# Kernel tuning notes

Measured on AMD Instinct MI355X. Metric: run time of the kernel, lower is better.

Reference implementation:

```python
import jax, jax.numpy as jnp
import numpy as np

N, E, F, H, L, G, C = 50000, 800000, 64, 128, 4, 64, 10
GAMMA = 10.0  # Gaussian RBF width for centers in (0,1)
CENTERS = jnp.linspace(0.0, 1.0, H)


def _ssp(v):
    # shifted softplus, SchNet's nonlinearity
    return jax.nn.softplus(v) - 0.6931472


def setup_inputs() -> dict:
    key = jax.random.key(0)
    ks = jax.random.split(key, 20)

    def w(k, shape, fan_in):
        return (jax.random.normal(k, shape, dtype=jnp.float32) / np.sqrt(fan_in)).astype(jnp.float32)

    x = jax.random.normal(ks[0], (N, F), dtype=jnp.float32)
    edge_dist = jax.random.uniform(ks[1], (E,), dtype=jnp.float32)
    edge_src = jax.random.randint(ks[2], (E,), 0, N, dtype=jnp.int32)
    edge_dst = jax.random.randint(ks[3], (E,), 0, N, dtype=jnp.int32)
    graph_ids = jnp.sort(jax.random.randint(ks[4], (N,), 0, G, dtype=jnp.int32))

    return {
        "x": x, "edge_dist": edge_dist,
        "edge_src": edge_src, "edge_dst": edge_dst, "graph_ids": graph_ids,
        # first-layer node projection F->H, remaining layers H->H (stacked)
        "W1_0": w(ks[5], (F, H), F), "b1_0": jnp.zeros((H,), jnp.float32),
        "W1_rest": w(ks[6], (L - 1, H, H), H), "b1_rest": jnp.zeros((L - 1, H), jnp.float32),
        # filter-generating MLP on RBF features, per layer
        "Wf1": w(ks[7], (L, H, H), H), "bf1": jnp.zeros((L, H), jnp.float32),
        "Wf2": w(ks[8], (L, H, H), H), "bf2": jnp.zeros((L, H), jnp.float32),
        # output projection per layer
        "W2": w(ks[9], (L, H, H), H), "b2": jnp.zeros((L, H), jnp.float32),
        # readout FC
        "fc_w": w(ks[10], (H, C), H), "fc_b": jnp.zeros((C,), jnp.float32),
    }


def _schnet_conv(x, rbf, src, dst, W1, b1, Wf1, bf1, Wf2, bf2, W2, b2):
    # CFConv: project nodes, gate gathered source features with a distance
    # filter, scatter-sum to destinations, project out.
    filt = _ssp(rbf @ Wf1 + bf1) @ Wf2 + bf2          # [E, H]
    h = x @ W1 + b1                                    # [N, H]
    msg = h[src] * filt                                # [E, H] gather + gate
    agg = jax.ops.segment_sum(msg, dst, num_segments=N)  # [N, H] scatter-sum
    return agg @ W2 + b2


def reference(x, edge_dist, edge_src, edge_dst, graph_ids,
              W1_0, b1_0, W1_rest, b1_rest, Wf1, bf1, Wf2, bf2, W2, b2,
              fc_w, fc_b):
    # Gaussian radial basis expansion of edge distances, shared across layers
    rbf = jnp.exp(-GAMMA * (edge_dist[:, None] - CENTERS) ** 2)  # [E, H]

    h = jax.nn.relu(_schnet_conv(x, rbf, edge_src, edge_dst,
                                 W1_0, b1_0, Wf1[0], bf1[0], Wf2[0], bf2[0],
                                 W2[0], b2[0]))
    for i in range(L - 1):
        h = jax.nn.relu(_schnet_conv(h, rbf, edge_src, edge_dst,
                                     W1_rest[i], b1_rest[i],
                                     Wf1[i + 1], bf1[i + 1],
                                     Wf2[i + 1], bf2[i + 1],
                                     W2[i + 1], b2[i + 1]))

    # dgl.mean_nodes: per-graph mean over nodes
    sums = jax.ops.segment_sum(h, graph_ids, num_segments=G)           # [G, H]
    cnts = jax.ops.segment_sum(jnp.ones((N,), h.dtype), graph_ids, num_segments=G)
    pooled = sums / jnp.maximum(cnts, 1.0)[:, None]

    logits = pooled @ fc_w + fc_b                                       # [G, C]
    return jax.nn.log_softmax(logits, axis=1)
```

## Files before the change

### kernel.cpp

```cpp
#include <hip/hip_runtime.h>
#include <math.h>

#define NN 50000
#define EE 800000
#define FF 64
#define HH 128
#define LL 4
#define GG 64
#define CC 10
#define TT 512
#define BD 64
#define ABLK 1024
#define EPB 782
#define SEGC 192
#define SUBB 96
#define SRW 6250

#define PB_CVTW 8
#define PB_TAB ((TT / 16) * LL)
#define PB_CVTX (NN * FF / 4 / 256)
#define PB_PART ABLK

typedef unsigned short ushort_t;
typedef unsigned int uint_t;

typedef short s8v __attribute__((ext_vector_type(8)));
typedef float f32x4 __attribute__((ext_vector_type(4)));

__device__ inline ushort_t f2bf(float f) {
  uint_t u = __float_as_uint(f);
  uint_t r = (u + 0x7FFFu + ((u >> 16) & 1u)) >> 16;
  return (ushort_t)r;
}
__device__ inline float bf_lo(uint_t pair) { return __uint_as_float(pair << 16); }
__device__ inline float bf_hi(uint_t pair) { return __uint_as_float(pair & 0xFFFF0000u); }
__device__ inline float bf1f(ushort_t v) { return __uint_as_float(((uint_t)v) << 16); }

__global__ __launch_bounds__(256) void prep(
    const float* __restrict__ x, ushort_t* __restrict__ xb,
    const float* __restrict__ W1_0, const float* __restrict__ W1_rest,
    const float* __restrict__ W2, ushort_t* __restrict__ wt,
    const float* __restrict__ Wf1, const float* __restrict__ bf1,
    const float* __restrict__ Wf2, const float* __restrict__ bf2,
    ushort_t* __restrict__ tables,
    const int* __restrict__ dst, const int* __restrict__ src,
    const float* __restrict__ dist,
    uint2* __restrict__ seg, int* __restrict__ segcnt, int* __restrict__ bcnt,
    const int* __restrict__ gid, int* __restrict__ gcnt, float* __restrict__ gsum) {
  __shared__ float rbf[16][HH];
  __shared__ float hid[16][HH];
  __shared__ int lcnt[8];
  int tid = threadIdx.x;
  int b = blockIdx.x;

  if (b < PB_CVTW) {
    int mid = b;
    const float* srcm; int K;
    if (mid == 0) { srcm = W1_0; K = FF; }
    else if (mid < 4) { srcm = W1_rest + (size_t)(mid - 1) * HH * HH; K = HH; }
    else { srcm = W2 + (size_t)(mid - 4) * HH * HH; K = HH; }
    ushort_t* dstm = wt + (size_t)mid * HH * HH;
    for (int idx = tid; idx < K * HH; idx += 256) {
      int k = idx >> 7, n = idx & 127;
      dstm[n * K + k] = f2bf(srcm[idx]);
    }
  } else if (b < PB_CVTW + PB_TAB) {
    int bb = b - PB_CVTW;
    int l = bb & 3;
    int tb = (bb >> 2) * 16;
    int j = tid & 127;
    float c = j * (1.0f / (HH - 1));
#pragma unroll
    for (int tt2 = 0; tt2 < 16; ++tt2) {
      float d = (tb + tt2) * (1.0f / (TT - 1));
      float dd = d - c;
      rbf[tt2][j] = expf(-10.0f * dd * dd);
    }
    __syncthreads();
    const float* W1f = Wf1 + (size_t)l * HH * HH;
    float s[16];
    float bb1 = bf1[l * HH + j];
#pragma unroll
    for (int tt2 = 0; tt2 < 16; ++tt2) s[tt2] = bb1;
    for (int k = 0; k < HH; ++k) {
      float wk = W1f[(size_t)k * HH + j];
#pragma unroll
      for (int tt2 = 0; tt2 < 16; ++tt2) s[tt2] += rbf[tt2][k] * wk;
    }
#pragma unroll
    for (int tt2 = 0; tt2 < 16; ++tt2)
      hid[tt2][j] = fmaxf(s[tt2], 0.f) + log1pf(expf(-fabsf(s[tt2]))) - 0.6931472f;
    __syncthreads();
    const float* W2f = Wf2 + (size_t)l * HH * HH;
    float bb2 = bf2[l * HH + j];
#pragma unroll
    for (int tt2 = 0; tt2 < 16; ++tt2) s[tt2] = bb2;
    for (int k = 0; k < HH; ++k) {
      float wk = W2f[(size_t)k * HH + j];
#pragma unroll
      for (int tt2 = 0; tt2 < 16; ++tt2) s[tt2] += hid[tt2][k] * wk;
    }
    if (tid < 128) {
#pragma unroll
      for (int tt2 = 0; tt2 < 16; ++tt2)
        tables[((size_t)l * TT + tb + tt2) * HH + j] = f2bf(s[tt2]);
    }
  } else if (b < PB_CVTW + PB_TAB + PB_CVTX) {
    int i = (b - PB_CVTW - PB_TAB) * 256 + tid;
    const float4* x4 = (const float4*)x;
    float4 v = x4[i];
    union { ushort_t us[4]; uint2 u; } pk;
    pk.us[0] = f2bf(v.x); pk.us[1] = f2bf(v.y); pk.us[2] = f2bf(v.z); pk.us[3] = f2bf(v.w);
    *(uint2*)&xb[i * 4] = pk.u;
  } else if (b < PB_CVTW + PB_TAB + PB_CVTX + PB_PART) {
    int pb = b - PB_CVTW - PB_TAB - PB_CVTX;
    if (tid < 8) lcnt[tid] = 0;
    int z = pb * 49 + tid;
    if (tid < 49 && z < NN) bcnt[z] = 0;
    __syncthreads();
    int e0 = pb * EPB;
    int e1 = min(e0 + EPB, EE);
    for (int e = e0 + tid; e < e1; e += 256) {
      int d = __builtin_nontemporal_load(dst + e);
      int s = __builtin_nontemporal_load(src + e);
      float di = __builtin_nontemporal_load(dist + e);
      float u = di * (float)(TT - 1);
      int t0 = (int)(fminf(fmaxf(u, 0.f), (float)(TT - 1)) + 0.5f);
      if (t0 > TT - 1) t0 = TT - 1;
      int r = d / SRW;
      int pos = atomicAdd(&lcnt[r], 1);
      if (pos < SEGC)
        seg[((size_t)(r << 10) + pb) * SEGC + pos] =
            make_uint2((uint_t)d, ((uint_t)s << 9) | (uint_t)t0);
    }
    __syncthreads();
    if (tid < 8) segcnt[(tid << 10) + pb] = min(lcnt[tid], SEGC);
  } else {
    for (int i = tid; i < GG * HH; i += 256) gsum[i] = 0.f;
    if (tid < GG) {
      int g = tid;
      int lo = 0, hi = NN;
      while (lo < hi) { int m = (lo + hi) >> 1; if (gid[m] < g) lo = m + 1; else hi = m; }
      int b0 = lo;
      lo = 0; hi = NN;
      int g1 = g + 1;
      while (lo < hi) { int m = (lo + hi) >> 1; if (gid[m] < g1) lo = m + 1; else hi = m; }
      gcnt[g] = lo - b0;
    }
  }
}

__global__ __launch_bounds__(256) void scatter_edges(
    const uint2* __restrict__ seg, const int* __restrict__ segcnt,
    int* __restrict__ bcnt, uint_t* __restrict__ epad) {
  int r = blockIdx.x & 7;
  int sub = blockIdx.x >> 3;
  int tid = threadIdx.x;
  for (int b = sub; b < ABLK; b += SUBB) {
    int cnt = segcnt[(r << 10) + b];
    const uint_t* sp = (const uint_t*)(seg + ((size_t)(r << 10) + b) * SEGC);
    for (int i = tid; i < cnt; i += 256) {
      uint_t ex = __builtin_nontemporal_load(sp + i * 2);
      uint_t ey = __builtin_nontemporal_load(sp + i * 2 + 1);
      int slot = atomicAdd(&bcnt[ex], 1);
      if (slot < BD) epad[(size_t)ex * BD + slot] = ey;
    }
  }
}

__global__ __launch_bounds__(256) void gemm_mfma(
    const ushort_t* __restrict__ A, const ushort_t* __restrict__ WT,
    const float* __restrict__ bias, ushort_t* __restrict__ OUT,
    int K, int act) {
  int lane = threadIdx.x & 63;
  int wave = threadIdx.x >> 6;
  int m = lane & 15;
  int quad = lane >> 4;
  int rowbase = blockIdx.x * 16;
  int colbase = wave * 32;
  const ushort_t* arow = A + (size_t)(rowbase + m) * K;
  const ushort_t* brow0 = WT + (size_t)(colbase + m) * K;
  const ushort_t* brow1 = WT + (size_t)(colbase + 16 + m) * K;
  f32x4 acc0 = {0.f, 0.f, 0.f, 0.f};
  f32x4 acc1 = {0.f, 0.f, 0.f, 0.f};
  for (int kc = 0; kc < K; kc += 32) {
    int k = kc + quad * 8;
    union { uint4 u; s8v v; } a, b0, b1;
    a.u  = *(const uint4*)(arow + k);
    b0.u = *(const uint4*)(brow0 + k);
    b1.u = *(const uint4*)(brow1 + k);
    acc0 = __builtin_amdgcn_mfma_f32_16x16x32_bf16(a.v, b0.v, acc0, 0, 0, 0);
    acc1 = __builtin_amdgcn_mfma_f32_16x16x32_bf16(a.v, b1.v, acc1, 0, 0, 0);
  }
  float bb0 = bias[colbase + m];
  float bb1 = bias[colbase + 16 + m];
#pragma unroll
  for (int reg = 0; reg < 4; ++reg) {
    int row = rowbase + quad * 4 + reg;
    float v0 = acc0[reg] + bb0;
    float v1 = acc1[reg] + bb1;
    if (act) { v0 = fmaxf(v0, 0.f); v1 = fmaxf(v1, 0.f); }
    OUT[(size_t)row * HH + colbase + m] = f2bf(v0);
    OUT[(size_t)row * HH + colbase + 16 + m] = f2bf(v1);
  }
}

__global__ __launch_bounds__(256) void gemm2_mfma(
    const ushort_t* __restrict__ AGG,
    const ushort_t* __restrict__ WT2, const float* __restrict__ b2l,
    const ushort_t* __restrict__ WT1, const float* __restrict__ b1l,
    ushort_t* __restrict__ OUT) {
  __shared__ ushort_t T[16 * 128];
  int lane = threadIdx.x & 63;
  int wave = threadIdx.x >> 6;
  int m = lane & 15;
  int quad = lane >> 4;
  int rowbase = blockIdx.x * 16;
  int colbase = wave * 32;
  {
    const ushort_t* arow = AGG + (size_t)(rowbase + m) * HH;
    const ushort_t* brow0 = WT2 + (size_t)(colbase + m) * HH;
    const ushort_t* brow1 = WT2 + (size_t)(colbase + 16 + m) * HH;
    f32x4 acc0 = {0.f, 0.f, 0.f, 0.f};
    f32x4 acc1 = {0.f, 0.f, 0.f, 0.f};
    for (int kc = 0; kc < HH; kc += 32) {
      int k = kc + quad * 8;
      union { uint4 u; s8v v; } a, b0, b1;
      a.u  = *(const uint4*)(arow + k);
      b0.u = *(const uint4*)(brow0 + k);
      b1.u = *(const uint4*)(brow1 + k);
      acc0 = __builtin_amdgcn_mfma_f32_16x16x32_bf16(a.v, b0.v, acc0, 0, 0, 0);
      acc1 = __builtin_amdgcn_mfma_f32_16x16x32_bf16(a.v, b1.v, acc1, 0, 0, 0);
    }
    float bb0 = b2l[colbase + m];
    float bb1 = b2l[colbase + 16 + m];
#pragma unroll
    for (int reg = 0; reg < 4; ++reg) {
      int r = quad * 4 + reg;
      float v0 = fmaxf(acc0[reg] + bb0, 0.f);
      float v1 = fmaxf(acc1[reg] + bb1, 0.f);
      int c0 = colbase + m, c1 = colbase + 16 + m;
      T[r * 128 + (((c0 >> 3) ^ r) << 3) + (c0 & 7)] = f2bf(v0);
      T[r * 128 + (((c1 >> 3) ^ r) << 3) + (c1 & 7)] = f2bf(v1);
    }
  }
  __syncthreads();
  {
    const ushort_t* brow0 = WT1 + (size_t)(colbase + m) * HH;
    const ushort_t* brow1 = WT1 + (size_t)(colbase + 16 + m) * HH;
    f32x4 acc0 = {0.f, 0.f, 0.f, 0.f};
    f32x4 acc1 = {0.f, 0.f, 0.f, 0.f};
    for (int kc = 0; kc < HH; kc += 32) {
      int k0 = kc + quad * 8;
      int g = k0 >> 3;
      union { uint4 u; s8v v; } a, b0, b1;
      a.u = *(const uint4*)&T[m * 128 + ((g ^ m) << 3)];
      b0.u = *(const uint4*)(brow0 + k0);
      b1.u = *(const uint4*)(brow1 + k0);
      acc0 = __builtin_amdgcn_mfma_f32_16x16x32_bf16(a.v, b0.v, acc0, 0, 0, 0);
      acc1 = __builtin_amdgcn_mfma_f32_16x16x32_bf16(a.v, b1.v, acc1, 0, 0, 0);
    }
    float bb0 = b1l[colbase + m];
    float bb1 = b1l[colbase + 16 + m];
#pragma unroll
    for (int reg = 0; reg < 4; ++reg) {
      int row = rowbase + quad * 4 + reg;
      OUT[(size_t)row * HH + colbase + m] = f2bf(acc0[reg] + bb0);
      OUT[(size_t)row * HH + colbase + 16 + m] = f2bf(acc1[reg] + bb1);
    }
  }
}

__global__ __launch_bounds__(256) void edge_agg(
    const ushort_t* __restrict__ p, const ushort_t* __restrict__ table,
    const uint_t* __restrict__ epad, const int* __restrict__ bcnt,
    ushort_t* __restrict__ agg) {
  int v = (blockIdx.x << 2) + (threadIdx.x >> 6);
  int lane = threadIdx.x & 63;
  if (v >= NN) return;
  int n = min(bcnt[v], BD);
  uint_t ed = (lane < n) ? epad[(size_t)v * BD + lane] : 0u;
  float ax = 0.f, ay = 0.f;
  int i = 0;
  int n4 = n & ~3;
  for (; i < n4; i += 4) {
    uint_t e0 = __shfl(ed, i + 0), e1 = __shfl(ed, i + 1);
    uint_t e2 = __shfl(ed, i + 2), e3 = __shfl(ed, i + 3);
    const uint_t* P0 = (const uint_t*)(p + (size_t)(e0 >> 9) * HH);
    const uint_t* P1 = (const uint_t*)(p + (size_t)(e1 >> 9) * HH);
    const uint_t* P2 = (const uint_t*)(p + (size_t)(e2 >> 9) * HH);
    const uint_t* P3 = (const uint_t*)(p + (size_t)(e3 >> 9) * HH);
    const uint_t* T0 = (const uint_t*)(table + (size_t)(e0 & 511u) * HH);
    const uint_t* T1 = (const uint_t*)(table + (size_t)(e1 & 511u) * HH);
    const uint_t* T2 = (const uint_t*)(table + (size_t)(e2 & 511u) * HH);
    const uint_t* T3 = (const uint_t*)(table + (size_t)(e3 & 511u) * HH);
    uint_t pv0 = P0[lane], pv1 = P1[lane], pv2 = P2[lane], pv3 = P3[lane];
    uint_t f0 = T0[lane], f1 = T1[lane], f2 = T2[lane], f3 = T3[lane];
    ax += bf_lo(pv0) * bf_lo(f0); ay += bf_hi(pv0) * bf_hi(f0);
    ax += bf_lo(pv1) * bf_lo(f1); ay += bf_hi(pv1) * bf_hi(f1);
    ax += bf_lo(pv2) * bf_lo(f2); ay += bf_hi(pv2) * bf_hi(f2);
    ax += bf_lo(pv3) * bf_lo(f3); ay += bf_hi(pv3) * bf_hi(f3);
  }
  for (; i < n; ++i) {
    uint_t e = __shfl(ed, i);
    uint_t pv = ((const uint_t*)(p + (size_t)(e >> 9) * HH))[lane];
    uint_t f = ((const uint_t*)(table + (size_t)(e & 511u) * HH))[lane];
    ax += bf_lo(pv) * bf_lo(f);
    ay += bf_hi(pv) * bf_hi(f);
  }
  uint_t packed = (uint_t)f2bf(ax) | ((uint_t)f2bf(ay) << 16);
  ((uint_t*)agg)[(size_t)v * 64 + lane] = packed;
}

__global__ __launch_bounds__(128) void pool_kernel(const ushort_t* __restrict__ h, const int* __restrict__ gid,
                                                   float* __restrict__ gsum) {
  int j = threadIdx.x;
  int i0 = blockIdx.x * 128;
  int i1 = min(i0 + 128, NN);
  if (i0 >= NN) return;
  float acc = 0.f;
  int gcur = gid[i0];
  for (int i = i0; i < i1; ++i) {
    int g = gid[i];
    if (g != gcur) {
      atomicAdd(&gsum[gcur * HH + j], acc);
      acc = 0.f;
      gcur = g;
    }
    acc += bf1f(h[(size_t)i * HH + j]);
  }
  atomicAdd(&gsum[gcur * HH + j], acc);
}

__global__ __launch_bounds__(128) void final_kernel(const float* __restrict__ gsum, const int* __restrict__ gcnt,
                                                    const float* __restrict__ fc_w, const float* __restrict__ fc_b,
                                                    float* __restrict__ out) {
  int g = blockIdx.x, j = threadIdx.x;
  __shared__ float pooled[HH];
  __shared__ float logits[CC];
  __shared__ float lse;
  float cnt = fmaxf((float)gcnt[g], 1.0f);
  pooled[j] = gsum[g * HH + j] / cnt;
  __syncthreads();
  if (j < CC) {
    float s = fc_b[j];
    for (int k = 0; k < HH; ++k) s += pooled[k] * fc_w[k * CC + j];
    logits[j] = s;
  }
  __syncthreads();
  if (j == 0) {
    float m = -1e30f;
    for (int c = 0; c < CC; ++c) m = fmaxf(m, logits[c]);
    float s = 0.f;
    for (int c = 0; c < CC; ++c) s += expf(logits[c] - m);
    lse = m + logf(s);
  }
  __syncthreads();
  if (j < CC) out[g * CC + j] = logits[j] - lse;
}

extern "C" void kernel_launch(void* const* d_in, const int* in_sizes, int n_in,
                              void* d_out, int out_size, void* d_ws, size_t ws_size,
                              hipStream_t stream) {
  const float* x       = (const float*)d_in[0];
  const float* edist   = (const float*)d_in[1];
  const int*   esrc    = (const int*)d_in[2];
  const int*   edst    = (const int*)d_in[3];
  const int*   gid     = (const int*)d_in[4];
  const float* W1_0    = (const float*)d_in[5];
  const float* b1_0    = (const float*)d_in[6];
  const float* W1_rest = (const float*)d_in[7];
  const float* b1_rest = (const float*)d_in[8];
  const float* Wf1     = (const float*)d_in[9];
  const float* bf1     = (const float*)d_in[10];
  const float* Wf2     = (const float*)d_in[11];
  const float* bf2     = (const float*)d_in[12];
  const float* W2      = (const float*)d_in[13];
  const float* b2      = (const float*)d_in[14];
  const float* fc_w    = (const float*)d_in[15];
  const float* fc_b    = (const float*)d_in[16];
  float* out = (float*)d_out;

  char* ws = (char*)d_ws;
  size_t o = 0;
  auto alloc = [&](size_t bytes) {
    void* p = ws + o;
    o += (bytes + 255) & ~(size_t)255;
    return p;
  };
  ushort_t* tables = (ushort_t*)alloc(sizeof(ushort_t) * (size_t)LL * TT * HH);
  ushort_t* xb     = (ushort_t*)alloc(sizeof(ushort_t) * (size_t)NN * FF);
  ushort_t* wt     = (ushort_t*)alloc(sizeof(ushort_t) * 8 * HH * HH);
  ushort_t* pbuf   = (ushort_t*)alloc(sizeof(ushort_t) * (size_t)NN * HH);
  ushort_t* hbuf   = (ushort_t*)alloc(sizeof(ushort_t) * (size_t)NN * HH);
  ushort_t* aggbuf = (ushort_t*)alloc(sizeof(ushort_t) * (size_t)NN * HH);
  int*      bcnt   = (int*)alloc(sizeof(int) * NN);
  uint_t*   epad   = (uint_t*)alloc(sizeof(uint_t) * (size_t)NN * BD);
  uint2*    seg    = (uint2*)alloc(sizeof(uint2) * (size_t)8 * ABLK * SEGC);
  int*      segcnt = (int*)alloc(sizeof(int) * 8 * ABLK);
  float*    gsum   = (float*)alloc(sizeof(float) * GG * HH);
  int*      gcnt   = (int*)alloc(sizeof(int) * GG);

  const int prepBlocks = PB_CVTW + PB_TAB + PB_CVTX + PB_PART + 1;
  prep<<<prepBlocks, 256, 0, stream>>>(x, xb, W1_0, W1_rest, W2, wt,
                                       Wf1, bf1, Wf2, bf2, tables,
                                       edst, esrc, edist, seg, segcnt, bcnt,
                                       gid, gcnt, gsum);
  scatter_edges<<<8 * SUBB, 256, 0, stream>>>(seg, segcnt, bcnt, epad);

  const int gemmBlocks = NN / 16;
  gemm_mfma<<<gemmBlocks, 256, 0, stream>>>(xb, wt, b1_0, pbuf, FF, 0);
  for (int l = 0; l < LL; ++l) {
    edge_agg<<<(NN + 3) / 4, 256, 0, stream>>>(pbuf, tables + (size_t)l * TT * HH,
                                               epad, bcnt, aggbuf);
    if (l < LL - 1) {
      gemm2_mfma<<<gemmBlocks, 256, 0, stream>>>(aggbuf,
                                                 wt + (size_t)(4 + l) * HH * HH, b2 + (size_t)l * HH,
                                                 wt + (size_t)(1 + l) * HH * HH, b1_rest + (size_t)l * HH,
                                                 pbuf);
    } else {
      gemm_mfma<<<gemmBlocks, 256, 0, stream>>>(aggbuf, wt + (size_t)(4 + l) * HH * HH,
                                                b2 + (size_t)l * HH, hbuf, HH, 1);
    }
  }

  pool_kernel<<<(NN + 127) / 128, 128, 0, stream>>>(hbuf, gid, gsum);
  final_kernel<<<GG, 128, 0, stream>>>(gsum, gcnt, fc_w, fc_b, out);
}
```

Baseline: 463.3 us.

## Fuse all stages into one persistent cooperative kernel with grid-wide syncs

Result: slower. 1.453 ms (+213.6%).

```diff
diff --git a/kernel.cpp b/kernel.cpp
--- a/kernel.cpp
+++ b/kernel.cpp
@@ -1,5 +1,8 @@
 #include <hip/hip_runtime.h>
+#include <hip/hip_cooperative_groups.h>
 #include <math.h>
+
+namespace cg = cooperative_groups;
 
 #define NN 50000
 #define EE 800000
@@ -20,6 +23,7 @@
 #define PB_TAB ((TT / 16) * LL)
 #define PB_CVTX (NN * FF / 4 / 256)
 #define PB_PART ABLK
+#define PB_TOTAL (PB_CVTW + PB_TAB + PB_CVTX + PB_PART + 1)
 
 typedef unsigned short ushort_t;
 typedef unsigned int uint_t;
@@ -36,23 +40,20 @@
 __device__ inline float bf_hi(uint_t pair) { return __uint_as_float(pair & 0xFFFF0000u); }
 __device__ inline float bf1f(ushort_t v) { return __uint_as_float(((uint_t)v) << 16); }
 
-__global__ __launch_bounds__(256) void prep(
+
+__device__ inline void prep_block(
+    int b, int tid,
     const float* __restrict__ x, ushort_t* __restrict__ xb,
     const float* __restrict__ W1_0, const float* __restrict__ W1_rest,
     const float* __restrict__ W2, ushort_t* __restrict__ wt,
     const float* __restrict__ Wf1, const float* __restrict__ bf1,
     const float* __restrict__ Wf2, const float* __restrict__ bf2,
     ushort_t* __restrict__ tables,
-    const int* __restrict__ dst, const int* __restrict__ src,
-    const float* __restrict__ dist,
+    const int* __restrict__ edst, const int* __restrict__ esrc,
+    const float* __restrict__ edist,
     uint2* __restrict__ seg, int* __restrict__ segcnt, int* __restrict__ bcnt,
-    const int* __restrict__ gid, int* __restrict__ gcnt, float* __restrict__ gsum) {
-  __shared__ float rbf[16][HH];
-  __shared__ float hid[16][HH];
-  __shared__ int lcnt[8];
-  int tid = threadIdx.x;
-  int b = blockIdx.x;
-
+    const int* __restrict__ gid, int* __restrict__ gcnt, float* __restrict__ gsum,
+    float (*rbf)[HH], float (*hid)[HH], int* lcnt) {
   if (b < PB_CVTW) {
     int mid = b;
     const float* srcm; int K;
@@ -71,39 +72,39 @@
     int j = tid & 127;
     float c = j * (1.0f / (HH - 1));
 #pragma unroll
-    for (int tt2 = 0; tt2 < 16; ++tt2) {
-      float d = (tb + tt2) * (1.0f / (TT - 1));
+    for (int t2 = 0; t2 < 16; ++t2) {
+      float d = (tb + t2) * (1.0f / (TT - 1));
       float dd = d - c;
-      rbf[tt2][j] = expf(-10.0f * dd * dd);
+      rbf[t2][j] = expf(-10.0f * dd * dd);
     }
     __syncthreads();
     const float* W1f = Wf1 + (size_t)l * HH * HH;
     float s[16];
     float bb1 = bf1[l * HH + j];
 #pragma unroll
-    for (int tt2 = 0; tt2 < 16; ++tt2) s[tt2] = bb1;
+    for (int t2 = 0; t2 < 16; ++t2) s[t2] = bb1;
     for (int k = 0; k < HH; ++k) {
       float wk = W1f[(size_t)k * HH + j];
 #pragma unroll
-      for (int tt2 = 0; tt2 < 16; ++tt2) s[tt2] += rbf[tt2][k] * wk;
-    }
-#pragma unroll
-    for (int tt2 = 0; tt2 < 16; ++tt2)
-      hid[tt2][j] = fmaxf(s[tt2], 0.f) + log1pf(expf(-fabsf(s[tt2]))) - 0.6931472f;
+      for (int t2 = 0; t2 < 16; ++t2) s[t2] += rbf[t2][k] * wk;
+    }
+#pragma unroll
+    for (int t2 = 0; t2 < 16; ++t2)
+      hid[t2][j] = fmaxf(s[t2], 0.f) + log1pf(expf(-fabsf(s[t2]))) - 0.6931472f;
     __syncthreads();
     const float* W2f = Wf2 + (size_t)l * HH * HH;
     float bb2 = bf2[l * HH + j];
 #pragma unroll
-    for (int tt2 = 0; tt2 < 16; ++tt2) s[tt2] = bb2;
+    for (int t2 = 0; t2 < 16; ++t2) s[t2] = bb2;
     for (int k = 0; k < HH; ++k) {
       float wk = W2f[(size_t)k * HH + j];
 #pragma unroll
-      for (int tt2 = 0; tt2 < 16; ++tt2) s[tt2] += hid[tt2][k] * wk;
+      for (int t2 = 0; t2 < 16; ++t2) s[t2] += hid[t2][k] * wk;
     }
     if (tid < 128) {
 #pragma unroll
-      for (int tt2 = 0; tt2 < 16; ++tt2)
-        tables[((size_t)l * TT + tb + tt2) * HH + j] = f2bf(s[tt2]);
+      for (int t2 = 0; t2 < 16; ++t2)
+        tables[((size_t)l * TT + tb + t2) * HH + j] = f2bf(s[t2]);
     }
   } else if (b < PB_CVTW + PB_TAB + PB_CVTX) {
     int i = (b - PB_CVTW - PB_TAB) * 256 + tid;
@@ -121,9 +122,9 @@
     int e0 = pb * EPB;
     int e1 = min(e0 + EPB, EE);
     for (int e = e0 + tid; e < e1; e += 256) {
-      int d = __builtin_nontemporal_load(dst + e);
-      int s = __builtin_nontemporal_load(src + e);
-      float di = __builtin_nontemporal_load(dist + e);
+      int d = __builtin_nontemporal_load(edst + e);
+      int s = __builtin_nontemporal_load(esrc + e);
+      float di = __builtin_nontemporal_load(edist + e);
       float u = di * (float)(TT - 1);
       int t0 = (int)(fminf(fmaxf(u, 0.f), (float)(TT - 1)) + 0.5f);
       if (t0 > TT - 1) t0 = TT - 1;
@@ -150,34 +151,27 @@
   }
 }
 
-__global__ __launch_bounds__(256) void scatter_edges(
-    const uint2* __restrict__ seg, const int* __restrict__ segcnt,
+__device__ inline void scatter_vb(
+    int vb, int tid, const uint2* __restrict__ seg, const int* __restrict__ segcnt,
     int* __restrict__ bcnt, uint_t* __restrict__ epad) {
-  int r = blockIdx.x & 7;
-  int sub = blockIdx.x >> 3;
-  int tid = threadIdx.x;
-  for (int b = sub; b < ABLK; b += SUBB) {
-    int cnt = segcnt[(r << 10) + b];
-    const uint_t* sp = (const uint_t*)(seg + ((size_t)(r << 10) + b) * SEGC);
+  int r = vb & 7, sub = vb >> 3;
+  for (int bb = sub; bb < ABLK; bb += SUBB) {
+    int cnt = segcnt[(r << 10) + bb];
+    const uint_t* sp = (const uint_t*)(seg + ((size_t)(r << 10) + bb) * SEGC);
     for (int i = tid; i < cnt; i += 256) {
-      uint_t ex = __builtin_nontemporal_load(sp + i * 2);
-      uint_t ey = __builtin_nontemporal_load(sp + i * 2 + 1);
+      uint_t ex = sp[i * 2];
+      uint_t ey = sp[i * 2 + 1];
       int slot = atomicAdd(&bcnt[ex], 1);
       if (slot < BD) epad[(size_t)ex * BD + slot] = ey;
     }
   }
 }
 
-__global__ __launch_bounds__(256) void gemm_mfma(
-    const ushort_t* __restrict__ A, const ushort_t* __restrict__ WT,
-    const float* __restrict__ bias, ushort_t* __restrict__ OUT,
-    int K, int act) {
-  int lane = threadIdx.x & 63;
-  int wave = threadIdx.x >> 6;
-  int m = lane & 15;
-  int quad = lane >> 4;
-  int rowbase = blockIdx.x * 16;
-  int colbase = wave * 32;
+__device__ inline void gemm_tile(const ushort_t* __restrict__ A, const ushort_t* __restrict__ WT,
+                                 const float* __restrict__ bias, ushort_t* __restrict__ OUT,
+                                 int K, int act, int tile, int tid) {
+  int lane = tid & 63, wave = tid >> 6, m = lane & 15, quad = lane >> 4;
+  int rowbase = tile * 16, colbase = wave * 32;
   const ushort_t* arow = A + (size_t)(rowbase + m) * K;
   const ushort_t* brow0 = WT + (size_t)(colbase + m) * K;
   const ushort_t* brow1 = WT + (size_t)(colbase + 16 + m) * K;
@@ -205,18 +199,12 @@
   }
 }
 
-__global__ __launch_bounds__(256) void gemm2_mfma(
-    const ushort_t* __restrict__ AGG,
-    const ushort_t* __restrict__ WT2, const float* __restrict__ b2l,
-    const ushort_t* __restrict__ WT1, const float* __restrict__ b1l,
-    ushort_t* __restrict__ OUT) {
-  __shared__ ushort_t T[16 * 128];
-  int lane = threadIdx.x & 63;
-  int wave = threadIdx.x >> 6;
-  int m = lane & 15;
-  int quad = lane >> 4;
-  int rowbase = blockIdx.x * 16;
-  int colbase = wave * 32;
+__device__ inline void gemm2_tile(const ushort_t* __restrict__ AGG,
+                                  const ushort_t* __restrict__ WT2, const float* __restrict__ b2l,
+                                  const ushort_t* __restrict__ WT1, const float* __restrict__ b1l,
+                                  ushort_t* __restrict__ OUT, int tile, int tid, ushort_t* T) {
+  int lane = tid & 63, wave = tid >> 6, m = lane & 15, quad = lane >> 4;
+  int rowbase = tile * 16, colbase = wave * 32;
   {
     const ushort_t* arow = AGG + (size_t)(rowbase + m) * HH;
     const ushort_t* brow0 = WT2 + (size_t)(colbase + m) * HH;
@@ -269,14 +257,15 @@
       OUT[(size_t)row * HH + colbase + 16 + m] = f2bf(acc1[reg] + bb1);
     }
   }
-}
-
-__global__ __launch_bounds__(256) void edge_agg(
-    const ushort_t* __restrict__ p, const ushort_t* __restrict__ table,
+  __syncthreads();
+}
+
+__device__ inline void edge_group(
+    int vg, int tid, const ushort_t* __restrict__ p, const ushort_t* __restrict__ tab,
     const uint_t* __restrict__ epad, const int* __restrict__ bcnt,
     ushort_t* __restrict__ agg) {
-  int v = (blockIdx.x << 2) + (threadIdx.x >> 6);
-  int lane = threadIdx.x & 63;
+  int v = (vg << 2) + (tid >> 6);
+  int lane = tid & 63;
   if (v >= NN) return;
   int n = min(bcnt[v], BD);
   uint_t ed = (lane < n) ? epad[(size_t)v * BD + lane] : 0u;
@@ -290,10 +279,10 @@
     const uint_t* P1 = (const uint_t*)(p + (size_t)(e1 >> 9) * HH);
     const uint_t* P2 = (const uint_t*)(p + (size_t)(e2 >> 9) * HH);
     const uint_t* P3 = (const uint_t*)(p + (size_t)(e3 >> 9) * HH);
-    const uint_t* T0 = (const uint_t*)(table + (size_t)(e0 & 511u) * HH);
-    const uint_t* T1 = (const uint_t*)(table + (size_t)(e1 & 511u) * HH);
-    const uint_t* T2 = (const uint_t*)(table + (size_t)(e2 & 511u) * HH);
-    const uint_t* T3 = (const uint_t*)(table + (size_t)(e3 & 511u) * HH);
+    const uint_t* T0 = (const uint_t*)(tab + (size_t)(e0 & 511u) * HH);
+    const uint_t* T1 = (const uint_t*)(tab + (size_t)(e1 & 511u) * HH);
+    const uint_t* T2 = (const uint_t*)(tab + (size_t)(e2 & 511u) * HH);
+    const uint_t* T3 = (const uint_t*)(tab + (size_t)(e3 & 511u) * HH);
     uint_t pv0 = P0[lane], pv1 = P1[lane], pv2 = P2[lane], pv3 = P3[lane];
     uint_t f0 = T0[lane], f1 = T1[lane], f2 = T2[lane], f3 = T3[lane];
     ax += bf_lo(pv0) * bf_lo(f0); ay += bf_hi(pv0) * bf_hi(f0);
@@ -304,7 +293,7 @@
   for (; i < n; ++i) {
     uint_t e = __shfl(ed, i);
     uint_t pv = ((const uint_t*)(p + (size_t)(e >> 9) * HH))[lane];
-    uint_t f = ((const uint_t*)(table + (size_t)(e & 511u) * HH))[lane];
+    uint_t f = ((const uint_t*)(tab + (size_t)(e & 511u) * HH))[lane];
     ax += bf_lo(pv) * bf_lo(f);
     ay += bf_hi(pv) * bf_hi(f);
   }
@@ -312,12 +301,13 @@
   ((uint_t*)agg)[(size_t)v * 64 + lane] = packed;
 }
 
-__global__ __launch_bounds__(128) void pool_kernel(const ushort_t* __restrict__ h, const int* __restrict__ gid,
-                                                   float* __restrict__ gsum) {
-  int j = threadIdx.x;
-  int i0 = blockIdx.x * 128;
+__device__ inline void pool_vb(int vb, int tid, const ushort_t* __restrict__ h,
+                               const int* __restrict__ gid, float* __restrict__ gsum) {
+  int strip = vb * 2 + (tid >> 7);
+  int j = tid & 127;
+  int i0 = strip * 128;
+  if (i0 >= NN) return;
   int i1 = min(i0 + 128, NN);
-  if (i0 >= NN) return;
   float acc = 0.f;
   int gcur = gid[i0];
   for (int i = i0; i < i1; ++i) {
@@ -332,31 +322,148 @@
   atomicAdd(&gsum[gcur * HH + j], acc);
 }
 
-__global__ __launch_bounds__(128) void final_kernel(const float* __restrict__ gsum, const int* __restrict__ gcnt,
-                                                    const float* __restrict__ fc_w, const float* __restrict__ fc_b,
-                                                    float* __restrict__ out) {
-  int g = blockIdx.x, j = threadIdx.x;
+__device__ inline void final_graph(int g, int tid, const float* __restrict__ gsum,
+                                   const int* __restrict__ gcnt,
+                                   const float* __restrict__ fc_w, const float* __restrict__ fc_b,
+                                   float* __restrict__ out,
+                                   float* pooled, float* logits, float* lse) {
+  if (tid < HH) pooled[tid] = gsum[g * HH + tid] / fmaxf((float)gcnt[g], 1.0f);
+  __syncthreads();
+  if (tid < CC) {
+    float s = fc_b[tid];
+    for (int k = 0; k < HH; ++k) s += pooled[k] * fc_w[k * CC + tid];
+    logits[tid] = s;
+  }
+  __syncthreads();
+  if (tid == 0) {
+    float mx = -1e30f;
+    for (int c2 = 0; c2 < CC; ++c2) mx = fmaxf(mx, logits[c2]);
+    float s = 0.f;
+    for (int c2 = 0; c2 < CC; ++c2) s += expf(logits[c2] - mx);
+    *lse = mx + logf(s);
+  }
+  __syncthreads();
+  if (tid < CC) out[g * CC + tid] = logits[tid] - *lse;
+  __syncthreads();
+}
+
+__global__ __launch_bounds__(256, 4) void mega(
+    const float* __restrict__ x, ushort_t* __restrict__ xb,
+    const float* __restrict__ W1_0, const float* __restrict__ W1_rest,
+    const float* __restrict__ W2, ushort_t* __restrict__ wt,
+    const float* __restrict__ Wf1, const float* __restrict__ bf1,
+    const float* __restrict__ Wf2, const float* __restrict__ bf2,
+    ushort_t* __restrict__ tables,
+    const int* __restrict__ edst, const int* __restrict__ esrc,
+    const float* __restrict__ edist,
+    uint2* __restrict__ seg, int* __restrict__ segcnt, int* __restrict__ bcnt,
+    uint_t* __restrict__ epad,
+    const int* __restrict__ gid, int* __restrict__ gcnt, float* __restrict__ gsum,
+    ushort_t* __restrict__ pbuf, ushort_t* __restrict__ hbuf, ushort_t* __restrict__ aggbuf,
+    const float* __restrict__ b1_0, const float* __restrict__ b1_rest,
+    const float* __restrict__ b2,
+    const float* __restrict__ fc_w, const float* __restrict__ fc_b,
+    float* __restrict__ out) {
+  cg::grid_group grid = cg::this_grid();
+  const int tid = threadIdx.x;
+  const int nb = gridDim.x;
+
+  __shared__ union {
+    struct { float rbf[16][HH]; float hid[16][HH]; int lcnt[8]; } prep;
+    ushort_t T[16 * 128];
+    struct { float pooled[HH]; float logits[CC]; float lse; } fin;
+  } sh;
+
+  for (int b = blockIdx.x; b < PB_TOTAL; b += nb) {
+    prep_block(b, tid, x, xb, W1_0, W1_rest, W2, wt, Wf1, bf1, Wf2, bf2, tables,
+               edst, esrc, edist, seg, segcnt, bcnt, gid, gcnt, gsum,
+               sh.prep.rbf, sh.prep.hid, sh.prep.lcnt);
+    __syncthreads();
+  }
+  grid.sync();
+
+  for (int vb = blockIdx.x; vb < 8 * SUBB; vb += nb)
+    scatter_vb(vb, tid, seg, segcnt, bcnt, epad);
+  grid.sync();
+
+  for (int t = blockIdx.x; t < NN / 16; t += nb)
+    gemm_tile(xb, wt, b1_0, pbuf, FF, 0, t, tid);
+
+  for (int l = 0; l < LL; ++l) {
+    grid.sync();
+    const ushort_t* tab = tables + (size_t)l * TT * HH;
+    for (int vg = blockIdx.x; vg < (NN + 3) / 4; vg += nb)
+      edge_group(vg, tid, pbuf, tab, epad, bcnt, aggbuf);
+    grid.sync();
+    if (l < LL - 1) {
+      for (int t = blockIdx.x; t < NN / 16; t += nb)
+        gemm2_tile(aggbuf, wt + (size_t)(4 + l) * HH * HH, b2 + (size_t)l * HH,
+                   wt + (size_t)(1 + l) * HH * HH, b1_rest + (size_t)l * HH,
+                   pbuf, t, tid, sh.T);
+    } else {
+      for (int t = blockIdx.x; t < NN / 16; t += nb)
+        gemm_tile(aggbuf, wt + (size_t)(4 + l) * HH * HH, b2 + (size_t)l * HH,
+                  hbuf, HH, 1, t, tid);
+    }
+  }
+  grid.sync();
+
+  for (int vb = blockIdx.x; vb < 196; vb += nb)
+    pool_vb(vb, tid, hbuf, gid, gsum);
+  grid.sync();
+
+  for (int g = blockIdx.x; g < GG; g += nb)
+    final_graph(g, tid, gsum, gcnt, fc_w, fc_b, out,
+                sh.fin.pooled, sh.fin.logits, &sh.fin.lse);
+}
+
+__global__ __launch_bounds__(256) void k_prep(
+    const float* x, ushort_t* xb, const float* W1_0, const float* W1_rest,
+    const float* W2, ushort_t* wt, const float* Wf1, const float* bf1,
+    const float* Wf2, const float* bf2, ushort_t* tables,
+    const int* edst, const int* esrc, const float* edist,
+    uint2* seg, int* segcnt, int* bcnt,
+    const int* gid, int* gcnt, float* gsum) {
+  __shared__ float rbf[16][HH];
+  __shared__ float hid[16][HH];
+  __shared__ int lcnt[8];
+  prep_block(blockIdx.x, threadIdx.x, x, xb, W1_0, W1_rest, W2, wt, Wf1, bf1, Wf2, bf2,
+             tables, edst, esrc, edist, seg, segcnt, bcnt, gid, gcnt, gsum, rbf, hid, lcnt);
+}
+
+__global__ __launch_bounds__(256) void k_scatter(const uint2* seg, const int* segcnt,
+                                                 int* bcnt, uint_t* epad) {
+  scatter_vb(blockIdx.x, threadIdx.x, seg, segcnt, bcnt, epad);
+}
+
+__global__ __launch_bounds__(256) void k_gemm(const ushort_t* A, const ushort_t* WT,
+                                              const float* bias, ushort_t* OUT, int K, int act) {
+  gemm_tile(A, WT, bias, OUT, K, act, blockIdx.x, threadIdx.x);
+}
+
+__global__ __launch_bounds__(256) void k_gemm2(const ushort_t* AGG, const ushort_t* WT2,
+                                               const float* b2l, const ushort_t* WT1,
+                                               const float* b1l, ushort_t* OUT) {
+  __shared__ ushort_t T[16 * 128];
+  gemm2_tile(AGG, WT2, b2l, WT1, b1l, OUT, blockIdx.x, threadIdx.x, T);
+}
+
+__global__ __launch_bounds__(256) void k_edge(const ushort_t* p, const ushort_t* tab,
+                                              const uint_t* epad, const int* bcnt,
+                                              ushort_t* agg) {
+  edge_group(blockIdx.x, threadIdx.x, p, tab, epad, bcnt, agg);
+}
+
+__global__ __launch_bounds__(256) void k_pool(const ushort_t* h, const int* gid, float* gsum) {
+  pool_vb(blockIdx.x, threadIdx.x, h, gid, gsum);
+}
+
+__global__ __launch_bounds__(256) void k_final(const float* gsum, const int* gcnt,
+                                               const float* fc_w, const float* fc_b, float* out) {
   __shared__ float pooled[HH];
   __shared__ float logits[CC];
   __shared__ float lse;
-  float cnt = fmaxf((float)gcnt[g], 1.0f);
-  pooled[j] = gsum[g * HH + j] / cnt;
-  __syncthreads();
-  if (j < CC) {
-    float s = fc_b[j];
-    for (int k = 0; k < HH; ++k) s += pooled[k] * fc_w[k * CC + j];
-    logits[j] = s;
-  }
-  __syncthreads();
-  if (j == 0) {
-    float m = -1e30f;
-    for (int c = 0; c < CC; ++c) m = fmaxf(m, logits[c]);
-    float s = 0.f;
-    for (int c = 0; c < CC; ++c) s += expf(logits[c] - m);
-    lse = m + logf(s);
-  }
-  __syncthreads();
-  if (j < CC) out[g * CC + j] = logits[j] - lse;
+  final_graph(blockIdx.x, threadIdx.x, gsum, gcnt, fc_w, fc_b, out, pooled, logits, &lse);
 }
 
 extern "C" void kernel_launch(void* const* d_in, const int* in_sizes, int n_in,
@@ -401,29 +508,50 @@
   float*    gsum   = (float*)alloc(sizeof(float) * GG * HH);
   int*      gcnt   = (int*)alloc(sizeof(int) * GG);
 
-  const int prepBlocks = PB_CVTW + PB_TAB + PB_CVTX + PB_PART + 1;
-  prep<<<prepBlocks, 256, 0, stream>>>(x, xb, W1_0, W1_rest, W2, wt,
-                                       Wf1, bf1, Wf2, bf2, tables,
-                                       edst, esrc, edist, seg, segcnt, bcnt,
-                                       gid, gcnt, gsum);
-  scatter_edges<<<8 * SUBB, 256, 0, stream>>>(seg, segcnt, bcnt, epad);
-
-  const int gemmBlocks = NN / 16;
-  gemm_mfma<<<gemmBlocks, 256, 0, stream>>>(xb, wt, b1_0, pbuf, FF, 0);
-  for (int l = 0; l < LL; ++l) {
-    edge_agg<<<(NN + 3) / 4, 256, 0, stream>>>(pbuf, tables + (size_t)l * TT * HH,
+  int dev = 0;
+  (void)hipGetDevice(&dev);
+  int coopAttr = 0;
+  (void)hipDeviceGetAttribute(&coopAttr, hipDeviceAttributeCooperativeLaunch, dev);
+  int nCU = 0;
+  (void)hipDeviceGetAttribute(&nCU, hipDeviceAttributeMultiprocessorCount, dev);
+  int occ = 0;
+  (void)hipOccupancyMaxActiveBlocksPerMultiprocessor(&occ, mega, 256, 0);
+
+  if (coopAttr && occ >= 1 && nCU > 0) {
+    int gridN = occ * nCU;
+    if (gridN > 1024) gridN = 1024;
+    void* args[] = {
+      (void*)&x, (void*)&xb, (void*)&W1_0, (void*)&W1_rest, (void*)&W2, (void*)&wt,
+      (void*)&Wf1, (void*)&bf1, (void*)&Wf2, (void*)&bf2, (void*)&tables,
+      (void*)&edst, (void*)&esrc, (void*)&edist,
+      (void*)&seg, (void*)&segcnt, (void*)&bcnt, (void*)&epad,
+      (void*)&gid, (void*)&gcnt, (void*)&gsum,
+      (void*)&pbuf, (void*)&hbuf, (void*)&aggbuf,
+      (void*)&b1_0, (void*)&b1_rest, (void*)&b2,
+      (void*)&fc_w, (void*)&fc_b, (void*)&out
+    };
+    (void)hipLaunchCooperativeKernel(mega, dim3(gridN), dim3(256), (void**)args, 0, stream);
+  } else {
+    k_prep<<<PB_TOTAL, 256, 0, stream>>>(x, xb, W1_0, W1_rest, W2, wt, Wf1, bf1, Wf2, bf2,
+                                         tables, edst, esrc, edist, seg, segcnt, bcnt,
+                                         gid, gcnt, gsum);
+    k_scatter<<<8 * SUBB, 256, 0, stream>>>(seg, segcnt, bcnt, epad);
+    const int gemmBlocks = NN / 16;
+    k_gemm<<<gemmBlocks, 256, 0, stream>>>(xb, wt, b1_0, pbuf, FF, 0);
+    for (int l = 0; l < LL; ++l) {
+      k_edge<<<(NN + 3) / 4, 256, 0, stream>>>(pbuf, tables + (size_t)l * TT * HH,
                                                epad, bcnt, aggbuf);
-    if (l < LL - 1) {
-      gemm2_mfma<<<gemmBlocks, 256, 0, stream>>>(aggbuf,
-                                                 wt + (size_t)(4 + l) * HH * HH, b2 + (size_t)l * HH,
-                                                 wt + (size_t)(1 + l) * HH * HH, b1_rest + (size_t)l * HH,
-                                                 pbuf);
-    } else {
-      gemm_mfma<<<gemmBlocks, 256, 0, stream>>>(aggbuf, wt + (size_t)(4 + l) * HH * HH,
-                                                b2 + (size_t)l * HH, hbuf, HH, 1);
-    }
-  }
-
-  pool_kernel<<<(NN + 127) / 128, 128, 0, stream>>>(hbuf, gid, gsum);
-  final_kernel<<<GG, 128, 0, stream>>>(gsum, gcnt, fc_w, fc_b, out);
-}
+      if (l < LL - 1) {
+        k_gemm2<<<gemmBlocks, 256, 0, stream>>>(aggbuf,
+                                                wt + (size_t)(4 + l) * HH * HH, b2 + (size_t)l * HH,
+                                                wt + (size_t)(1 + l) * HH * HH, b1_rest + (size_t)l * HH,
+                                                pbuf);
+      } else {
+        k_gemm<<<gemmBlocks, 256, 0, stream>>>(aggbuf, wt + (size_t)(4 + l) * HH * HH,
+                                               b2 + (size_t)l * HH, hbuf, HH, 1);
+      }
+    }
+    k_pool<<<196, 256, 0, stream>>>(hbuf, gid, gsum);
+    k_final<<<GG, 256, 0, stream>>>(gsum, gcnt, fc_w, fc_b, out);
+  }
+}
```
